# Optimization experiments

Measured on AMD Instinct MI355X. Metric: run time of the kernel, lower is better.

## Reference

```python
import jax, jax.numpy as jnp
from jax import lax
import numpy as np

H = 64  # hidden size

def lstm_layer(x, w_ih, w_hh, b_ih, b_hh):
    # x: [B,T,I]; w_ih: [4H,I]; w_hh: [4H,H]; gates ordered i,f,g,o (PyTorch)
    B = x.shape[0]
    xg = jnp.einsum('bti,gi->btg', x, w_ih) + b_ih  # precompute input projections [B,T,4H]
    h0 = jnp.zeros((B, H), x.dtype)
    c0 = jnp.zeros((B, H), x.dtype)
    def step(carry, xt):
        h, c = carry
        gates = xt + h @ w_hh.T + b_hh
        i, f, g, o = jnp.split(gates, 4, axis=-1)
        c = jax.nn.sigmoid(f) * c + jax.nn.sigmoid(i) * jnp.tanh(g)
        h = jax.nn.sigmoid(o) * jnp.tanh(c)
        return (h, c), h
    (hT, cT), hs = lax.scan(step, (h0, c0), jnp.swapaxes(xg, 0, 1))
    return jnp.swapaxes(hs, 0, 1), hT, cT

def layernorm(x, g, b, eps=1e-5):
    mu = jnp.mean(x, axis=-1, keepdims=True)
    var = jnp.mean(jnp.square(x - mu), axis=-1, keepdims=True)
    return (x - mu) * lax.rsqrt(var + eps) * g + b

def setup_inputs() -> dict:
    key = jax.random.key(0)
    ks = jax.random.split(key, 16)
    s = 0.05
    return {
        'x': jax.random.normal(ks[0], (512, 1024, 32), jnp.float32),
        'w_ih1': jax.random.normal(ks[1], (4 * H, 32)) * s,
        'w_hh1': jax.random.normal(ks[2], (4 * H, H)) * s,
        'b_ih1': jax.random.normal(ks[3], (4 * H,)) * s,
        'b_hh1': jax.random.normal(ks[4], (4 * H,)) * s,
        'w_ih2': jax.random.normal(ks[5], (4 * H, H)) * s,
        'w_hh2': jax.random.normal(ks[6], (4 * H, H)) * s,
        'b_ih2': jax.random.normal(ks[7], (4 * H,)) * s,
        'b_hh2': jax.random.normal(ks[8], (4 * H,)) * s,
        'fc1_w': jax.random.normal(ks[9], (128, H)) * s,
        'fc1_b': jax.random.normal(ks[10], (128,)) * s,
        'fc2_w': jax.random.normal(ks[11], (128, 128)) * s,
        'fc2_b': jax.random.normal(ks[12], (128,)) * s,
        'ln_g': jnp.ones((128,), jnp.float32),
        'ln_b': jnp.zeros((128,), jnp.float32),
    }

def reference(x, w_ih1, w_hh1, b_ih1, b_hh1, w_ih2, w_hh2, b_ih2, b_hh2,
              fc1_w, fc1_b, fc2_w, fc2_b, ln_g, ln_b):
    h1, _, _ = lstm_layer(x, w_ih1, w_hh1, b_ih1, b_hh1)
    # dropout(0.1) is identity in eval mode
    _, hT, _ = lstm_layer(h1, w_ih2, w_hh2, b_ih2, b_hh2)
    y = jax.nn.relu(hT @ fc1_w.T + fc1_b)
    y = y @ fc2_w.T + fc2_b
    return layernorm(y, ln_g, ln_b)
```

## Files before the change

### kernel.cpp

```cpp
#include <hip/hip_runtime.h>
#include <cstdint>
#include <cstddef>

#define T_STEPS 1024
#define SEG     16
#define NSEG    (T_STEPS / SEG)
#define NBLK    256
#define LOG2E   1.4426950408889634f

typedef __attribute__((ext_vector_type(8))) _Float16 half8;
typedef __attribute__((ext_vector_type(4))) float    f32x4;
typedef __attribute__((ext_vector_type(4))) int      i32x4;

static __device__ __forceinline__ float fexp2(float x) {
#if defined(__has_builtin) && __has_builtin(__builtin_amdgcn_exp2f)
  return __builtin_amdgcn_exp2f(x);
#else
  return __exp2f(x);
#endif
}
static __device__ __forceinline__ float sigm2(float a) {
  return __builtin_amdgcn_rcpf(1.0f + fexp2(-a));
}
static __device__ __forceinline__ float tanhg2(float a) {
  return 2.0f * __builtin_amdgcn_rcpf(1.0f + fexp2(-(a + a))) - 1.0f;
}
static __device__ __forceinline__ float tanhc127(float c) {
  return 127.0f - 254.0f * __builtin_amdgcn_rcpf(1.0f + fexp2(c * (2.0f * LOG2E)));
}

static __device__ __forceinline__ half8 load8s(const float* s, float sc) {
  float4 a = ((const float4*)s)[0];
  float4 b = ((const float4*)s)[1];
  half8 h;
  h[0] = (_Float16)(a.x * sc); h[1] = (_Float16)(a.y * sc);
  h[2] = (_Float16)(a.z * sc); h[3] = (_Float16)(a.w * sc);
  h[4] = (_Float16)(b.x * sc); h[5] = (_Float16)(b.y * sc);
  h[6] = (_Float16)(b.z * sc); h[7] = (_Float16)(b.w * sc);
  return h;
}
static __device__ __forceinline__ i32x4 quant16(const float* src, float s) {
  union { i32x4 v; signed char b[16]; } u;
  #pragma unroll
  for (int j = 0; j < 16; ++j) u.b[j] = (signed char)__float2int_rn(src[j] * s);
  return u.v;
}

static __device__ __forceinline__ void barrier_lds() {
  __asm__ volatile("s_waitcnt lgkmcnt(0)\n\ts_barrier" ::: "memory");
}

__global__ __launch_bounds__(512, 2) void lstm_fused(
    const float* __restrict__ x,
    const float* __restrict__ w_ih1, const float* __restrict__ w_hh1,
    const float* __restrict__ b_ih1, const float* __restrict__ b_hh1,
    const float* __restrict__ w_ih2, const float* __restrict__ w_hh2,
    const float* __restrict__ b_ih2, const float* __restrict__ b_hh2,
    const float* __restrict__ fc1_w, const float* __restrict__ fc1_b,
    const float* __restrict__ fc2_w, const float* __restrict__ fc2_b,
    const float* __restrict__ ln_g, const float* __restrict__ ln_b,
    float* __restrict__ out)
{
  __shared__ __align__(16) signed char h1ring[32][2][64];
  __shared__ __align__(16) signed char h2ring[2][2][64];
  __shared__ __align__(16) float xg1b[2][SEG][2][64][4];
  __shared__ __align__(16) float xg2b[2][SEG][2][64][4];
  __shared__ __align__(16) float hfin[2][64];
  __shared__ __align__(16) float y1s[2][128];
  __shared__ __align__(16) float y2s[2][128];
  __shared__ float redmu[2], redrs[2];

  const int t   = threadIdx.x;
  const int blk = blockIdx.x;
  const int l   = t & 63;
  const int w   = t >> 6;
  const int col = l & 15;
  const int q   = l >> 4;
  const int myb = w & 1;
  const int kbase = (w & 1) * 2;

  ((int*)h1ring)[t]       = 0;
  ((int*)h1ring)[t + 512] = 0;
  if (t < 64) ((int*)h2ring)[t] = 0;

  const i32x4 zi = (i32x4){0, 0, 0, 0};
  f32x4 zf; zf[0] = 0.f; zf[1] = 0.f; zf[2] = 0.f; zf[3] = 0.f;

  i32x4 wq[4][4];
  i32x4 wq2[4][2];
  half8 wbx[4][2];
  f32x4 fsa;
  float fsx[4][2];
  float bL[4][2];

  if (w < 4) {
    const float* W = (w < 2) ? w_hh1 : w_hh2;
    float fsq[4][4];
    #pragma unroll
    for (int g = 0; g < 4; ++g) {
      #pragma unroll
      for (int k = 0; k < 4; ++k) {
        const int r = g * 64 + k * 16 + col;
        const float* p = W + r * 64 + q * 16;
        float m = 0.0f;
        #pragma unroll
        for (int j = 0; j < 16; ++j) m = fmaxf(m, fabsf(p[j]));
        m = fmaxf(m, __shfl_xor(m, 16, 64));
        m = fmaxf(m, __shfl_xor(m, 32, 64));
        wq[g][k] = quant16(p, 127.0f / m);
        fsq[g][k] = m * (LOG2E / 16129.0f);
      }
    }
    #pragma unroll
    for (int g = 0; g < 4; ++g) {
      const float v01 = (q & 1) ? fsq[g][1] : fsq[g][0];
      const float v23 = (q & 1) ? fsq[g][3] : fsq[g][2];
      fsa[g] = (q & 2) ? v23 : v01;
    }
  } else if (w < 6) {
    #pragma unroll
    for (int g = 0; g < 4; ++g) {
      #pragma unroll
      for (int k2 = 0; k2 < 2; ++k2) {
        const int r = g * 64 + (kbase + k2) * 16 + col;
        const float* p = w_ih2 + r * 64 + q * 16;
        float m = 0.0f;
        #pragma unroll
        for (int j = 0; j < 16; ++j) m = fmaxf(m, fabsf(p[j]));
        m = fmaxf(m, __shfl_xor(m, 16, 64));
        m = fmaxf(m, __shfl_xor(m, 32, 64));
        wq2[g][k2] = quant16(p, 127.0f / m);
        fsx[g][k2] = m * (LOG2E / 16129.0f);
        bL[g][k2]  = (b_ih2[r] + b_hh2[r]) * LOG2E;
      }
    }
  } else {
    #pragma unroll
    for (int g = 0; g < 4; ++g) {
      #pragma unroll
      for (int k2 = 0; k2 < 2; ++k2) {
        const int r = g * 64 + (kbase + k2) * 16 + col;
        wbx[g][k2] = load8s(w_ih1 + r * 32 + q * 8, LOG2E);
        bL[g][k2]  = (b_ih1[r] + b_hh1[r]) * LOG2E;
      }
    }
  }

  const int tl  = (l & 15) >> 1;
  const int axb = l & 1;

  float c = 0.0f;

  auto produce_xg1 = [&](int tau) {
    float* dst = &xg1b[tau & 1][0][0][0][0];
    #pragma unroll
    for (int h8 = 0; h8 < 2; ++h8) {
      const float* xs = x + ((size_t)(2 * blk + axb) * T_STEPS +
                             (tau * SEG + h8 * 8 + tl)) * 32 + q * 8;
      const float4 va = ((const float4*)xs)[0];
      const float4 vb = ((const float4*)xs)[1];
      half8 xf;
      xf[0] = (_Float16)va.x; xf[1] = (_Float16)va.y;
      xf[2] = (_Float16)va.z; xf[3] = (_Float16)va.w;
      xf[4] = (_Float16)vb.x; xf[5] = (_Float16)vb.y;
      xf[6] = (_Float16)vb.z; xf[7] = (_Float16)vb.w;
      f32x4 accf[4][2];
      #pragma unroll
      for (int g = 0; g < 4; ++g)
        #pragma unroll
        for (int k2 = 0; k2 < 2; ++k2)
          accf[g][k2] = __builtin_amdgcn_mfma_f32_16x16x32_f16(xf, wbx[g][k2], zf, 0, 0, 0);
      #pragma unroll
      for (int k2 = 0; k2 < 2; ++k2) {
        #pragma unroll
        for (int r = 0; r < 4; ++r) {
          const int row = h8 * 16 + q * 4 + r;
          f32x4 v;
          v[0] = accf[0][k2][r] + bL[0][k2];
          v[1] = accf[1][k2][r] + bL[1][k2];
          v[2] = accf[2][k2][r] + bL[2][k2];
          v[3] = accf[3][k2][r] + bL[3][k2];
          *(f32x4*)(dst + (size_t)(row * 64 + (kbase + k2) * 16 + col) * 4) = v;
        }
      }
    }
  };

  auto produce_xg2 = [&](int sg) {
    float* dst = &xg2b[sg & 1][0][0][0][0];
    #pragma unroll
    for (int h8 = 0; h8 < 2; ++h8) {
      const i32x4 a = *(const i32x4*)((const signed char*)h1ring +
                      (size_t)((((sg * SEG + h8 * 8 + tl) & 31) * 128) + axb * 64 + q * 16));
      i32x4 acc[4][2];
      #pragma unroll
      for (int g = 0; g < 4; ++g)
        #pragma unroll
        for (int k2 = 0; k2 < 2; ++k2)
          acc[g][k2] = __builtin_amdgcn_mfma_i32_16x16x64_i8(a, wq2[g][k2], zi, 0, 0, 0);
      #pragma unroll
      for (int k2 = 0; k2 < 2; ++k2) {
        #pragma unroll
        for (int r = 0; r < 4; ++r) {
          const int row = h8 * 16 + q * 4 + r;
          f32x4 v;
          v[0] = bL[0][k2] + fsx[0][k2] * (float)acc[0][k2][r];
          v[1] = bL[1][k2] + fsx[1][k2] * (float)acc[1][k2][r];
          v[2] = bL[2][k2] + fsx[2][k2] * (float)acc[2][k2][r];
          v[3] = bL[3][k2] + fsx[3][k2] * (float)acc[3][k2][r];
          *(f32x4*)(dst + (size_t)(row * 64 + (kbase + k2) * 16 + col) * 4) = v;
        }
      }
    }
  };

  auto run_seg = [&](const float* XG, signed char* RING, int RM, int t0, bool fin) {
    f32x4 xq[8];
    #pragma unroll
    for (int j = 0; j < 8; ++j)
      xq[j] = *(const f32x4*)(XG + (size_t)((j * 2 + myb) * 64 + l) * 4);
    __builtin_amdgcn_s_setprio(1);
    #pragma unroll
    for (int j8 = 0; j8 < SEG; ++j8) {
      const int tt = t0 + j8;
      const i32x4 a = *(const i32x4*)(RING + ((tt - 1) & RM) * 128 + myb * 64 + q * 16);
      const f32x4 xv = xq[j8 & 7];
      if (j8 < 8)
        xq[j8 & 7] = *(const f32x4*)(XG + (size_t)(((j8 + 8) * 2 + myb) * 64 + l) * 4);
      i32x4 acc[4][4];
      #pragma unroll
      for (int g = 0; g < 4; ++g)
        #pragma unroll
        for (int k = 0; k < 4; ++k)
          acc[g][k] = __builtin_amdgcn_mfma_i32_16x16x64_i8(a, wq[g][k], zi, 0, 0, 0);
      float p[4];
      #pragma unroll
      for (int g = 0; g < 4; ++g) {
        const int a01 = (q & 1) ? acc[g][1][0] : acc[g][0][0];
        const int a23 = (q & 1) ? acc[g][3][0] : acc[g][2][0];
        const int ai  = (q & 2) ? a23 : a01;
        p[g] = xv[g] + fsa[g] * (float)ai;
      }
      const float gi = sigm2(p[0]), gf = sigm2(p[1]);
      const float gg = tanhg2(p[2]), go = sigm2(p[3]);
      c = gf * c + gi * gg;
      const float hq = go * tanhc127(c);
      RING[(tt & RM) * 128 + myb * 64 + l] = (signed char)__float2int_rn(hq);
      if (fin && j8 == SEG - 1) hfin[myb][l] = hq * (1.0f / 127.0f);
    }
    __builtin_amdgcn_s_setprio(0);
  };

  if (w >= 6) produce_xg1(0);
  barrier_lds();

  for (int s = 0; s <= NSEG + 1; ++s) {
    if (w < 2) {
      if (s < NSEG)
        run_seg(&xg1b[s & 1][0][0][0][0], (signed char*)h1ring, 31, s * SEG, false);
    } else if (w < 4) {
      const int sg = s - 2;
      if (sg >= 0)
        run_seg(&xg2b[sg & 1][0][0][0][0], (signed char*)h2ring, 1, sg * SEG,
                sg == NSEG - 1);
    } else if (w < 6) {
      const int sg = s - 1;
      if (sg >= 0 && sg < NSEG) produce_xg2(sg);
    } else {
      if (s + 1 < NSEG) produce_xg1(s + 1);
    }
    barrier_lds();
  }

  __syncthreads();

  if (t < 256) {
    const int bi = t >> 7, j = t & 127;
    float accv = fc1_b[j];
    const float4* w4 = (const float4*)(fc1_w + j * 64);
    const float4* h4 = (const float4*)hfin[bi];
    #pragma unroll
    for (int qq = 0; qq < 16; ++qq) {
      float4 wv = w4[qq]; float4 hv = h4[qq];
      accv += wv.x * hv.x + wv.y * hv.y + wv.z * hv.z + wv.w * hv.w;
    }
    y1s[bi][j] = fmaxf(accv, 0.0f);
  }
  __syncthreads();
  if (t < 256) {
    const int bi = t >> 7, j = t & 127;
    float accv = fc2_b[j];
    const float4* w4 = (const float4*)(fc2_w + j * 128);
    const float4* y4 = (const float4*)y1s[bi];
    #pragma unroll
    for (int qq = 0; qq < 32; ++qq) {
      float4 wv = w4[qq]; float4 yv = y4[qq];
      accv += wv.x * yv.x + wv.y * yv.y + wv.z * yv.z + wv.w * yv.w;
    }
    y2s[bi][j] = accv;
  }
  __syncthreads();
  if (t < 128) {
    const int bi = t >> 6, jj = t & 63;
    float s  = y2s[bi][jj] + y2s[bi][64 + jj];
    float qs = y2s[bi][jj] * y2s[bi][jj] + y2s[bi][64 + jj] * y2s[bi][64 + jj];
    #pragma unroll
    for (int off = 32; off > 0; off >>= 1) {
      s  += __shfl_down(s, off, 64);
      qs += __shfl_down(qs, off, 64);
    }
    if (jj == 0) {
      const float mu  = s * (1.0f / 128.0f);
      const float var = qs * (1.0f / 128.0f) - mu * mu;
      redmu[bi] = mu;
      redrs[bi] = rsqrtf(var + 1e-5f);
    }
  }
  __syncthreads();
  if (t < 256) {
    const int bi = t >> 7, j = t & 127;
    out[(size_t)(2 * blk + bi) * 128 + j] =
        (y2s[bi][j] - redmu[bi]) * redrs[bi] * ln_g[j] + ln_b[j];
  }
}

extern "C" void kernel_launch(void* const* d_in, const int* in_sizes, int n_in,
                              void* d_out, int out_size, void* d_ws, size_t ws_size,
                              hipStream_t stream) {
  const float* x     = (const float*)d_in[0];
  const float* w_ih1 = (const float*)d_in[1];
  const float* w_hh1 = (const float*)d_in[2];
  const float* b_ih1 = (const float*)d_in[3];
  const float* b_hh1 = (const float*)d_in[4];
  const float* w_ih2 = (const float*)d_in[5];
  const float* w_hh2 = (const float*)d_in[6];
  const float* b_ih2 = (const float*)d_in[7];
  const float* b_hh2 = (const float*)d_in[8];
  const float* fc1_w = (const float*)d_in[9];
  const float* fc1_b = (const float*)d_in[10];
  const float* fc2_w = (const float*)d_in[11];
  const float* fc2_b = (const float*)d_in[12];
  const float* ln_g  = (const float*)d_in[13];
  const float* ln_b  = (const float*)d_in[14];
  float* out = (float*)d_out;

  lstm_fused<<<NBLK, 512, 0, stream>>>(x, w_ih1, w_hh1, b_ih1, b_hh1,
                                       w_ih2, w_hh2, b_ih2, b_hh2,
                                       fc1_w, fc1_b, fc2_w, fc2_b,
                                       ln_g, ln_b, out);
}
```

Measured before the change: 409.1 us.

## Exchange recurrent h via DPP and ds_bpermute instead of LDS ring round-trip

The recurrent hidden state is no longer written to an LDS ring and read back each step. Each lane now packs its int8 h bytes with DPP moves and redistributes them with ds_bpermute straight into the MFMA A-operand register. The h1 ring is still written because the layer-2 input projection reads it, while the layer-2 ring is dropped. The gate math is also folded to share reciprocals (sigmoid*tanh products computed with one rcp each), cutting transcendental count on the serial critical path. The packing shifts and permute indexing assume a specific MFMA operand layout, so a layout mismatch would be a correctness risk.

```diff
diff --git a/kernel.cpp b/kernel.cpp
--- a/kernel.cpp
+++ b/kernel.cpp
@@ -18,15 +18,6 @@
 #else
   return __exp2f(x);
 #endif
-}
-static __device__ __forceinline__ float sigm2(float a) {
-  return __builtin_amdgcn_rcpf(1.0f + fexp2(-a));
-}
-static __device__ __forceinline__ float tanhg2(float a) {
-  return 2.0f * __builtin_amdgcn_rcpf(1.0f + fexp2(-(a + a))) - 1.0f;
-}
-static __device__ __forceinline__ float tanhc127(float c) {
-  return 127.0f - 254.0f * __builtin_amdgcn_rcpf(1.0f + fexp2(c * (2.0f * LOG2E)));
 }
 
 static __device__ __forceinline__ half8 load8s(const float* s, float sc) {
@@ -62,7 +53,6 @@
     float* __restrict__ out)
 {
   __shared__ __align__(16) signed char h1ring[32][2][64];
-  __shared__ __align__(16) signed char h2ring[2][2][64];
   __shared__ __align__(16) float xg1b[2][SEG][2][64][4];
   __shared__ __align__(16) float xg2b[2][SEG][2][64][4];
   __shared__ __align__(16) float hfin[2][64];
@@ -81,7 +71,6 @@
 
   ((int*)h1ring)[t]       = 0;
   ((int*)h1ring)[t + 512] = 0;
-  if (t < 64) ((int*)h2ring)[t] = 0;
 
   const i32x4 zi = (i32x4){0, 0, 0, 0};
   f32x4 zf; zf[0] = 0.f; zf[1] = 0.f; zf[2] = 0.f; zf[3] = 0.f;
@@ -149,7 +138,14 @@
   const int tl  = (l & 15) >> 1;
   const int axb = l & 1;
 
-  float c = 0.0f;
+  float c  = 0.0f;
+  i32x4 af = zi;
+  const int sh1 = (l & 1) << 3;
+  const int sh2 = (l & 2) << 3;
+  const int bpa0 = ((q << 4) + 0 + (l & 3)) << 2;
+  const int bpa1 = ((q << 4) + 4 + (l & 3)) << 2;
+  const int bpa2 = ((q << 4) + 8 + (l & 3)) << 2;
+  const int bpa3 = ((q << 4) + 12 + (l & 3)) << 2;
 
   auto produce_xg1 = [&](int tau) {
     float* dst = &xg1b[tau & 1][0][0][0][0];
@@ -214,7 +210,7 @@
     }
   };
 
-  auto run_seg = [&](const float* XG, signed char* RING, int RM, int t0, bool fin) {
+  auto run_seg = [&](const float* XG, int t0, bool ring, bool fin) {
     f32x4 xq[8];
     #pragma unroll
     for (int j = 0; j < 8; ++j)
@@ -223,7 +219,6 @@
     #pragma unroll
     for (int j8 = 0; j8 < SEG; ++j8) {
       const int tt = t0 + j8;
-      const i32x4 a = *(const i32x4*)(RING + ((tt - 1) & RM) * 128 + myb * 64 + q * 16);
       const f32x4 xv = xq[j8 & 7];
       if (j8 < 8)
         xq[j8 & 7] = *(const f32x4*)(XG + (size_t)(((j8 + 8) * 2 + myb) * 64 + l) * 4);
@@ -232,7 +227,7 @@
       for (int g = 0; g < 4; ++g)
         #pragma unroll
         for (int k = 0; k < 4; ++k)
-          acc[g][k] = __builtin_amdgcn_mfma_i32_16x16x64_i8(a, wq[g][k], zi, 0, 0, 0);
+          acc[g][k] = __builtin_amdgcn_mfma_i32_16x16x64_i8(af, wq[g][k], zi, 0, 0, 0);
       float p[4];
       #pragma unroll
       for (int g = 0; g < 4; ++g) {
@@ -241,12 +236,33 @@
         const int ai  = (q & 2) ? a23 : a01;
         p[g] = xv[g] + fsa[g] * (float)ai;
       }
-      const float gi = sigm2(p[0]), gf = sigm2(p[1]);
-      const float gg = tanhg2(p[2]), go = sigm2(p[3]);
-      c = gf * c + gi * gg;
-      const float hq = go * tanhc127(c);
-      RING[(tt & RM) * 128 + myb * 64 + l] = (signed char)__float2int_rn(hq);
+      const float Ei = fexp2(-p[0]);
+      const float Ef = fexp2(-p[1]);
+      const float Eg = fexp2(-(p[2] + p[2]));
+      const float Eo = fexp2(-p[3]);
+      const float gf = __builtin_amdgcn_rcpf(1.0f + Ef);
+      const float ig = (1.0f - Eg) *
+                       __builtin_amdgcn_rcpf((1.0f + Ei) * (1.0f + Eg));
+      c = gf * c + ig;
+      const float E  = fexp2(c * (2.0f * LOG2E));
+      const float hq = fmaf(127.0f, E, -127.0f) *
+                       __builtin_amdgcn_rcpf((1.0f + Eo) * (1.0f + E));
+      const int  B  = __float2int_rn(hq) & 255;
+      if (ring)
+        ((signed char*)h1ring)[(tt & 31) * 128 + myb * 64 + l] = (signed char)B;
       if (fin && j8 == SEG - 1) hfin[myb][l] = hq * (1.0f / 127.0f);
+      const int a1 = B << sh1;
+      const int t1 = __builtin_amdgcn_mov_dpp(a1, 0xB1, 0xF, 0xF, false);
+      const int u2 = a1 | t1;
+      const int a2 = u2 << sh2;
+      const int t2 = __builtin_amdgcn_mov_dpp(a2, 0x4E, 0xF, 0xF, false);
+      const int D  = a2 | t2;
+      i32x4 nf;
+      nf[0] = __builtin_amdgcn_ds_bpermute(bpa0, D);
+      nf[1] = __builtin_amdgcn_ds_bpermute(bpa1, D);
+      nf[2] = __builtin_amdgcn_ds_bpermute(bpa2, D);
+      nf[3] = __builtin_amdgcn_ds_bpermute(bpa3, D);
+      af = nf;
     }
     __builtin_amdgcn_s_setprio(0);
   };
@@ -257,12 +273,11 @@
   for (int s = 0; s <= NSEG + 1; ++s) {
     if (w < 2) {
       if (s < NSEG)
-        run_seg(&xg1b[s & 1][0][0][0][0], (signed char*)h1ring, 31, s * SEG, false);
+        run_seg(&xg1b[s & 1][0][0][0][0], s * SEG, true, false);
     } else if (w < 4) {
       const int sg = s - 2;
       if (sg >= 0)
-        run_seg(&xg2b[sg & 1][0][0][0][0], (signed char*)h2ring, 1, sg * SEG,
-                sg == NSEG - 1);
+        run_seg(&xg2b[sg & 1][0][0][0][0], sg * SEG, false, sg == NSEG - 1);
     } else if (w < 6) {
       const int sg = s - 1;
       if (sg >= 0 && sg < NSEG) produce_xg2(sg);
```

Result: slower. 430.6 us (+5.3%).
